# Optimization experiments

Measured on AMD Instinct MI355X. Metric: run time of the kernel, lower is better.

The kernel has to match this reference:

```python
import jax, jax.numpy as jnp
import numpy as np
from jax import lax

_MS_SSIM_WEIGHTS = [0.0448, 0.2856, 0.3001, 0.2363, 0.1333]
LEVELS = 5
WINDOW_SIZE = 11
SIGMA = 1.5
DATA_RANGE = 2.0


def _gaussian_kernel(size, sigma, channels):
    x = jnp.arange(size, dtype=jnp.float32) - size // 2
    g = jnp.exp(-x ** 2 / (2.0 * sigma ** 2))
    g = g / g.sum()
    k2d = jnp.outer(g, g)  # [size, size]
    # depthwise kernel: [C, 1, size, size] (OIHW with feature_group_count=C)
    return jnp.broadcast_to(k2d[None, None], (channels, 1, size, size))


def _depthwise_conv(x, kernel, pad):
    C = x.shape[1]
    return lax.conv_general_dilated(
        x, kernel,
        window_strides=(1, 1),
        padding=[(pad, pad), (pad, pad)],
        dimension_numbers=('NCHW', 'OIHW', 'NCHW'),
        feature_group_count=C)


def _avg_pool2(x):
    s = lax.reduce_window(x, 0.0, lax.add, (1, 1, 2, 2), (1, 1, 2, 2), 'VALID')
    return s * 0.25


def _ssim(x, y, window_size=WINDOW_SIZE, sigma=SIGMA, data_range=DATA_RANGE):
    K1, K2 = 0.01, 0.03
    C1 = (K1 * data_range) ** 2
    C2 = (K2 * data_range) ** 2
    kernel = _gaussian_kernel(window_size, sigma, x.shape[1])
    pad = window_size // 2
    mu1 = _depthwise_conv(x, kernel, pad)
    mu2 = _depthwise_conv(y, kernel, pad)
    mu1_sq = mu1 * mu1
    mu2_sq = mu2 * mu2
    mu1_mu2 = mu1 * mu2
    sig1_sq = _depthwise_conv(x * x, kernel, pad) - mu1_sq
    sig2_sq = _depthwise_conv(y * y, kernel, pad) - mu2_sq
    sig12 = _depthwise_conv(x * y, kernel, pad) - mu1_mu2
    num = (2.0 * mu1_mu2 + C1) * (2.0 * sig12 + C2)
    den = (mu1_sq + mu2_sq + C1) * (sig1_sq + sig2_sq + C2)
    ssim_map = num / (den + 1e-8)
    return ssim_map.mean()


def setup_inputs() -> dict:
    key = jax.random.key(0)
    k1, k2 = jax.random.split(key)
    pred = jax.random.normal(k1, (16, 3, 512, 512), dtype=jnp.float32)
    target = jax.random.normal(k2, (16, 3, 512, 512), dtype=jnp.float32)
    return {"pred": pred, "target": target}


def reference(pred, target):
    weights = jnp.asarray(_MS_SSIM_WEIGHTS[:LEVELS], dtype=jnp.float32)
    weights = weights / weights.sum()
    ms_ssim_val = jnp.zeros((), dtype=jnp.float32)
    x, y = pred, target
    for i in range(LEVELS):
        s = _ssim(x, y)
        ms_ssim_val = ms_ssim_val + weights[i] * s
        if i < LEVELS - 1:
            x = _avg_pool2(x)
            y = _avg_pool2(y)
    return 1.0 - ms_ssim_val
```

## Files before the change

kernel.cpp:

```cpp
#include <hip/hip_runtime.h>


#define TW 64
#define NIMG 48
#define P2 63
#define P1 62
#define NSLOT 256
#define SSTRIDE 16

typedef float v2f __attribute__((ext_vector_type(2)));

template <int TH>
__global__ __launch_bounds__(256, 2) void ssim_level_kernel(
    const float* __restrict__ x, const float* __restrict__ y,
    long imgStride, int rowStride,
    float* __restrict__ dsx, float* __restrict__ dsy,
    long dsImgStride, int dsRowStride,
    const float* __restrict__ zpad,
    float* __restrict__ slots, int H, int W, int pad, int do_ds)
{
    constexpr int HHALO = TH + 10;
    constexpr int RPT   = TH / 4;

    const float G[11] = {
        0.00102839f, 0.00759877f, 0.03600077f, 0.10936069f, 0.21300539f,
        0.26601173f, 0.21300539f, 0.10936069f, 0.03600077f, 0.00759877f,
        0.00102839f};
    const float C1 = 4.0e-4f;
    const float C2 = 3.6e-3f;

    __shared__ __align__(16) v2f   sm01[HHALO * P2];
    __shared__ __align__(16) v2f   sm23[HHALO * P2];
    __shared__ __align__(16) float sm4 [HHALO * P1];

    const int t   = threadIdx.x;
    const int img = blockIdx.z;
    const int C0  = blockIdx.x * TW;
    const int R0  = blockIdx.y * TH;
    const float* xi = x + (long)img * imgStride;
    const float* yi = y + (long)img * imgStride;

    if (do_ds) {
        const int dsW = W >> 1, dsH = H >> 1;
        const long dbase = (long)img * dsImgStride;
        for (int i = t; i < (TH / 2) * 32; i += 256) {
            const int dr = i >> 5, dc = i & 31;
            const int gr2 = (R0 >> 1) + dr;
            const int gc2 = (C0 >> 1) + dc;
            if (gr2 < dsH && gc2 < dsW) {
                const float* sx = xi + (long)(2 * gr2) * rowStride + 2 * gc2;
                const float* sy = yi + (long)(2 * gr2) * rowStride + 2 * gc2;
                const float2 a0 = *reinterpret_cast<const float2*>(sx);
                const float2 a1 = *reinterpret_cast<const float2*>(sx + rowStride);
                const float2 b0 = *reinterpret_cast<const float2*>(sy);
                const float2 b1 = *reinterpret_cast<const float2*>(sy + rowStride);
                const long o = dbase + (long)gr2 * dsRowStride + gc2;
                dsx[o] = 0.25f * (a0.x + a0.y + a1.x + a1.y);
                dsy[o] = 0.25f * (b0.x + b0.y + b1.x + b1.y);
            }
            if (gr2 < dsH && dc < 8) {
                if (blockIdx.x == 0) {
                    const long o = dbase + (long)gr2 * dsRowStride + (dc - 8);
                    dsx[o] = 0.0f; dsy[o] = 0.0f;
                }
                if (blockIdx.x == gridDim.x - 1) {
                    const long o = dbase + (long)gr2 * dsRowStride + (dsW + dc);
                    dsx[o] = 0.0f; dsy[o] = 0.0f;
                }
            }
        }
    }

    const bool fastp = pad || ((C0 >= 8) && (C0 + TW + 8 <= W));
    for (int s = t; s < HHALO * 8; s += 256) {
        const int r  = s % HHALO;
        const int q  = s / HHALO;
        const int gr = R0 + r - 5;
        const bool rok = ((unsigned)gr < (unsigned)H);
        const int gc0 = C0 + (q << 3) - 8;

        float xv[24], yv[24];
        if (fastp) {
            const float* px = rok ? (xi + (long)gr * rowStride + gc0) : zpad;
            const float* py = rok ? (yi + (long)gr * rowStride + gc0) : zpad;
#pragma unroll
            for (int v = 0; v < 6; ++v) {
                const float4 a = reinterpret_cast<const float4*>(px)[v];
                const float4 b = reinterpret_cast<const float4*>(py)[v];
                xv[4 * v + 0] = a.x; xv[4 * v + 1] = a.y;
                xv[4 * v + 2] = a.z; xv[4 * v + 3] = a.w;
                yv[4 * v + 0] = b.x; yv[4 * v + 1] = b.y;
                yv[4 * v + 2] = b.z; yv[4 * v + 3] = b.w;
            }
        } else {
            const float* xrow = xi + (long)gr * rowStride;
            const float* yrow = yi + (long)gr * rowStride;
#pragma unroll
            for (int k = 3; k < 21; ++k) {
                const int gc = gc0 + k;
                const bool ok = rok && ((unsigned)gc < (unsigned)W);
                xv[k] = ok ? xrow[gc] : 0.0f;
                yv[k] = ok ? yrow[gc] : 0.0f;
            }
        }

        v2f w2[18]; float xy[18];
#pragma unroll
        for (int k = 0; k < 18; ++k) {
            const float a = xv[k + 3], b = yv[k + 3];
            v2f w; w.x = a * a; w.y = b * b;
            w2[k] = w; xy[k] = a * b;
        }

        const int cb = (q << 3);
#pragma unroll
        for (int j = 0; j < 8; ++j) {
            v2f s01 = {0.f, 0.f}, s23 = {0.f, 0.f};
            float s4 = 0.f;
#pragma unroll
            for (int k = 0; k < 11; ++k) {
                const float g = G[k];
                v2f w; w.x = xv[j + k + 3]; w.y = yv[j + k + 3];
                s01 += w * g;
                s23 += w2[j + k] * g;
                s4   = fmaf(g, xy[j + k], s4);
            }
            sm01[r * P2 + cb + j] = s01;
            sm23[r * P2 + cb + j] = s23;
            sm4 [r * P1 + cb + j] = s4;
        }
    }
    __syncthreads();

    const int c   = t & 63;
    const int rr0 = (t >> 6) * RPT;
    v2f acc01[RPT], acc23[RPT];
    float acc4[RPT];
    {
        v2f hv[RPT + 10];
#pragma unroll
        for (int k = 0; k < RPT + 10; ++k) hv[k] = sm01[(rr0 + k) * P2 + c];
#pragma unroll
        for (int i = 0; i < RPT; ++i) {
            v2f a = {0.f, 0.f};
#pragma unroll
            for (int k = 0; k < 11; ++k) a += hv[i + k] * G[k];
            acc01[i] = a;
        }
#pragma unroll
        for (int k = 0; k < RPT + 10; ++k) hv[k] = sm23[(rr0 + k) * P2 + c];
#pragma unroll
        for (int i = 0; i < RPT; ++i) {
            v2f a = {0.f, 0.f};
#pragma unroll
            for (int k = 0; k < 11; ++k) a += hv[i + k] * G[k];
            acc23[i] = a;
        }
    }
    {
        float hs[RPT + 10];
#pragma unroll
        for (int k = 0; k < RPT + 10; ++k) hs[k] = sm4[(rr0 + k) * P1 + c];
#pragma unroll
        for (int i = 0; i < RPT; ++i) {
            float a = 0.f;
#pragma unroll
            for (int k = 0; k < 11; ++k) a = fmaf(G[k], hs[i + k], a);
            acc4[i] = a;
        }
    }

    float local = 0.f;
    const int gc = C0 + c;
#pragma unroll
    for (int i = 0; i < RPT; ++i) {
        const int gr2 = R0 + rr0 + i;
        if (gr2 < H && gc < W) {
            const float mu1 = acc01[i].x, mu2 = acc01[i].y;
            const float mu1s = mu1 * mu1, mu2s = mu2 * mu2, m12 = mu1 * mu2;
            const float s1  = acc23[i].x - mu1s;
            const float s2  = acc23[i].y - mu2s;
            const float s12 = acc4[i] - m12;
            const float num = (2.f * m12 + C1) * (2.f * s12 + C2);
            const float den = (mu1s + mu2s + C1) * (s1 + s2 + C2);
            local += num * __builtin_amdgcn_rcpf(den + 1e-8f);
        }
    }

#pragma unroll
    for (int off = 32; off > 0; off >>= 1) local += __shfl_down(local, off, 64);
    if ((t & 63) == 0) {
        const int bid = (blockIdx.z * gridDim.y + blockIdx.y) * gridDim.x + blockIdx.x;
        const int slot = ((bid << 2) | (t >> 6)) & (NSLOT - 1);
        atomicAdd(slots + slot * SSTRIDE, local);
    }
}

__global__ void finalize_kernel(const float* __restrict__ slots,
                                float* __restrict__ out)
{
    const int t = threadIdx.x;
    const float w[5] = {0.0448f, 0.2856f, 0.3001f, 0.2363f, 0.1333f};
    const float wsum = w[0] + w[1] + w[2] + w[3] + w[4];
    float acc = 0.f;
#pragma unroll
    for (int lvl = 0; lvl < 5; ++lvl) {
        const int d = 512 >> lvl;
        const float cnt = (float)NIMG * (float)d * (float)d;
        acc += (w[lvl] / wsum) / cnt * slots[(lvl * NSLOT + t) * SSTRIDE];
    }
#pragma unroll
    for (int off = 32; off > 0; off >>= 1) acc += __shfl_down(acc, off, 64);
    __shared__ float p[4];
    if ((t & 63) == 0) p[t >> 6] = acc;
    __syncthreads();
    if (t == 0) out[0] = 1.0f - (p[0] + p[1] + p[2] + p[3]);
}

extern "C" void kernel_launch(void* const* d_in, const int* in_sizes, int n_in,
                              void* d_out, int out_size, void* d_ws, size_t ws_size,
                              hipStream_t stream)
{
    const float* pred = (const float*)d_in[0];
    const float* targ = (const float*)d_in[1];
    float* out = (float*)d_out;
    float* ws  = (float*)d_ws;

    const long S1 = 256L * 272, S2 = 128L * 144, S3 = 64L * 80, S4 = 32L * 48;

    float* slots = ws;
    float* zpad  = slots + 5 * NSLOT * SSTRIDE;
    float* x1 = zpad + 640;
    float* y1 = x1 + NIMG * S1;
    float* x2 = y1 + NIMG * S1;
    float* y2 = x2 + NIMG * S2;
    float* x3 = y2 + NIMG * S2;
    float* y3 = x3 + NIMG * S3;
    float* x4 = y3 + NIMG * S3;
    float* y4 = x4 + NIMG * S4;

    hipMemsetAsync(ws, 0, (size_t)(5 * NSLOT * SSTRIDE + 640) * sizeof(float), stream);

    { dim3 g(8, 16, NIMG);
      ssim_level_kernel<32><<<g, 256, 0, stream>>>(pred, targ, 512L * 512, 512,
          x1 + 8, y1 + 8, S1, 272, zpad, slots + 0 * NSLOT * SSTRIDE, 512, 512, 0, 1); }
    { dim3 g(4, 8, NIMG);
      ssim_level_kernel<32><<<g, 256, 0, stream>>>(x1 + 8, y1 + 8, S1, 272,
          x2 + 8, y2 + 8, S2, 144, zpad, slots + 1 * NSLOT * SSTRIDE, 256, 256, 1, 1); }
    { dim3 g(2, 16, NIMG);
      ssim_level_kernel<8><<<g, 256, 0, stream>>>(x2 + 8, y2 + 8, S2, 144,
          x3 + 8, y3 + 8, S3, 80, zpad, slots + 2 * NSLOT * SSTRIDE, 128, 128, 1, 1); }
    { dim3 g(1, 8, NIMG);
      ssim_level_kernel<8><<<g, 256, 0, stream>>>(x3 + 8, y3 + 8, S3, 80,
          x4 + 8, y4 + 8, S4, 48, zpad, slots + 3 * NSLOT * SSTRIDE, 64, 64, 1, 1); }
    { dim3 g(1, 4, NIMG);
      ssim_level_kernel<8><<<g, 256, 0, stream>>>(x4 + 8, y4 + 8, S4, 48,
          nullptr, nullptr, 0, 0, zpad, slots + 4 * NSLOT * SSTRIDE, 32, 32, 1, 0); }

    finalize_kernel<<<1, 256, 0, stream>>>(slots, out);
}
```

Baseline: 283.6 us.

## Add rolling-window SSIM kernel with ring-buffer horizontal pass for top two levels

```diff
diff --git a/kernel.cpp b/kernel.cpp
--- a/kernel.cpp
+++ b/kernel.cpp
@@ -3,12 +3,230 @@
 
 #define TW 64
 #define NIMG 48
+#define WIN 42
+#define PQ  64
+#define P4  65
 #define P2 63
 #define P1 62
 #define NSLOT 256
 #define SSTRIDE 16
 
 typedef float v2f __attribute__((ext_vector_type(2)));
+typedef float v4f __attribute__((ext_vector_type(4)));
+
+__device__ __forceinline__ void h_load(
+    const float* __restrict__ xi, const float* __restrict__ yi,
+    const float* __restrict__ zpad, int gr, int gc0, int H, int W,
+    bool fastp, int rowStride, float* xv, float* yv)
+{
+    const bool rok = ((unsigned)gr < (unsigned)H);
+    if (fastp) {
+        const float* px = rok ? (xi + (long)gr * rowStride + gc0) : zpad;
+        const float* py = rok ? (yi + (long)gr * rowStride + gc0) : zpad;
+#pragma unroll
+        for (int v = 0; v < 6; ++v) {
+            const float4 a = reinterpret_cast<const float4*>(px)[v];
+            const float4 b = reinterpret_cast<const float4*>(py)[v];
+            xv[4*v+0]=a.x; xv[4*v+1]=a.y; xv[4*v+2]=a.z; xv[4*v+3]=a.w;
+            yv[4*v+0]=b.x; yv[4*v+1]=b.y; yv[4*v+2]=b.z; yv[4*v+3]=b.w;
+        }
+    } else {
+        const float* xrow = xi + (long)gr * rowStride;
+        const float* yrow = yi + (long)gr * rowStride;
+#pragma unroll
+        for (int k = 3; k < 21; ++k) {
+            const int gc = gc0 + k;
+            const bool ok = rok && ((unsigned)gc < (unsigned)W);
+            xv[k] = ok ? xrow[gc] : 0.0f;
+            yv[k] = ok ? yrow[gc] : 0.0f;
+        }
+    }
+}
+
+__device__ __forceinline__ void h_conv_write(
+    const float* xv, const float* yv, v4f* smA, float* smB,
+    int slot, int cb, const float* G)
+{
+    v2f s01[8], s23[8];
+    float s4[8];
+#pragma unroll
+    for (int j = 0; j < 8; ++j) {
+        s01[j] = {0.f, 0.f}; s23[j] = {0.f, 0.f}; s4[j] = 0.f;
+    }
+#pragma unroll
+    for (int m = 0; m < 18; ++m) {
+        const float a = xv[m+3], b = yv[m+3];
+        v2f w;  w.x  = a;   w.y  = b;
+        v2f w2; w2.x = a*a; w2.y = b*b;
+        const float ab = a * b;
+#pragma unroll
+        for (int j = 0; j < 8; ++j) {
+            if (j <= m && m - j <= 10) {
+                const float g = G[m - j];
+                s01[j] += w * g;
+                s23[j] += w2 * g;
+                s4[j] = fmaf(g, ab, s4[j]);
+            }
+        }
+    }
+    const int u = slot & 31;
+#pragma unroll
+    for (int j = 0; j < 8; ++j) {
+        v4f o; o.x = s01[j].x; o.y = s01[j].y; o.z = s23[j].x; o.w = s23[j].y;
+        smA[slot * PQ + ((cb + j) ^ u)] = o;
+        smB[slot * P4 + cb + j] = s4[j];
+    }
+}
+
+template <int NSUB>
+__global__ __launch_bounds__(256, 3) void ssim_rolling_kernel(
+    const float* __restrict__ x, const float* __restrict__ y,
+    long imgStride, int rowStride,
+    float* __restrict__ dsx, float* __restrict__ dsy,
+    long dsImgStride, int dsRowStride,
+    const float* __restrict__ zpad,
+    float* __restrict__ slots, int H, int W, int pad, int do_ds)
+{
+    const float G[11] = {
+        0.00102839f, 0.00759877f, 0.03600077f, 0.10936069f, 0.21300539f,
+        0.26601173f, 0.21300539f, 0.10936069f, 0.03600077f, 0.00759877f,
+        0.00102839f};
+    const float C1 = 4.0e-4f;
+    const float C2 = 3.6e-3f;
+
+    __shared__ __align__(16) v4f smA[WIN * PQ];
+    __shared__ float             smB[WIN * P4];
+
+    const int t   = threadIdx.x;
+    const int img = blockIdx.z;
+    const int C0  = blockIdx.x * TW;
+    const int S0  = blockIdx.y * (NSUB * 32);
+    const float* xi = x + (long)img * imgStride;
+    const float* yi = y + (long)img * imgStride;
+    const bool fastp = pad || ((C0 >= 8) && (C0 + TW + 8 <= W));
+
+    for (int s = t; s < WIN * 8; s += 256) {
+        const int r = s % WIN, q = s / WIN;
+        float pxv[24], pyv[24];
+        h_load(xi, yi, zpad, S0 + r - 5, C0 + (q << 3) - 8, H, W, fastp,
+               rowStride, pxv, pyv);
+        h_conv_write(pxv, pyv, smA, smB, r, q << 3, G);
+    }
+    __syncthreads();
+
+    const int c   = t & 63;
+    const int rr0 = (t >> 6) * 8;
+    const int hr  = t & 31, hq = t >> 5;
+    const int hgc0 = C0 + (hq << 3) - 8;
+    int wslot = hr;
+    int vb    = rr0;
+    float local = 0.f;
+    const int dsW = W >> 1, dsH = H >> 1;
+    const long dbase = (long)img * dsImgStride;
+
+    float xv[24], yv[24];
+
+    for (int tt = 0; tt < NSUB; ++tt) {
+        const int R0 = S0 + 32 * tt;
+
+        if (tt < NSUB - 1)
+            h_load(xi, yi, zpad, R0 + 37 + hr, hgc0, H, W, fastp, rowStride,
+                   xv, yv);
+
+        float2 pa0[2], pa1[2], pb0[2], pb1[2];
+        if (do_ds) {
+#pragma unroll
+            for (int ii = 0; ii < 2; ++ii) {
+                const int i  = t + (ii << 8);
+                const int dr = i >> 5, dc = i & 31;
+                const int gr2 = (R0 >> 1) + dr, gc2 = (C0 >> 1) + dc;
+                if (gr2 < dsH && gc2 < dsW) {
+                    const float* sx = xi + (long)(2*gr2) * rowStride + 2*gc2;
+                    const float* sy = yi + (long)(2*gr2) * rowStride + 2*gc2;
+                    pa0[ii] = *reinterpret_cast<const float2*>(sx);
+                    pa1[ii] = *reinterpret_cast<const float2*>(sx + rowStride);
+                    pb0[ii] = *reinterpret_cast<const float2*>(sy);
+                    pb1[ii] = *reinterpret_cast<const float2*>(sy + rowStride);
+                }
+            }
+        }
+
+        v4f accA[8]; float acc4[8];
+#pragma unroll
+        for (int i = 0; i < 8; ++i) {
+            accA[i] = {0.f, 0.f, 0.f, 0.f}; acc4[i] = 0.f;
+        }
+        int sl = __builtin_amdgcn_readfirstlane(vb);
+#pragma unroll
+        for (int k = 0; k < 18; ++k) {
+            const v4f  h  = smA[sl * PQ + (c ^ (sl & 31))];
+            const float hb = smB[sl * P4 + c];
+#pragma unroll
+            for (int i = 0; i < 8; ++i) {
+                if (i <= k && k - i <= 10) {
+                    const float g = G[k - i];
+                    accA[i] += h * g;
+                    acc4[i] = fmaf(g, hb, acc4[i]);
+                }
+            }
+            sl = (sl + 1 == WIN) ? 0 : sl + 1;
+        }
+#pragma unroll
+        for (int i = 0; i < 8; ++i) {
+            const int gr2 = R0 + rr0 + i;
+            const int gc  = C0 + c;
+            if (gr2 < H && gc < W) {
+                const float mu1 = accA[i].x, mu2 = accA[i].y;
+                const float mu1s = mu1*mu1, mu2s = mu2*mu2, m12 = mu1*mu2;
+                const float s1  = accA[i].z - mu1s;
+                const float s2  = accA[i].w - mu2s;
+                const float s12 = acc4[i] - m12;
+                const float num = (2.f * m12 + C1) * (2.f * s12 + C2);
+                const float den = (mu1s + mu2s + C1) * (s1 + s2 + C2);
+                local += num * __builtin_amdgcn_rcpf(den + 1e-8f);
+            }
+        }
+        __syncthreads();
+
+        if (do_ds) {
+#pragma unroll
+            for (int ii = 0; ii < 2; ++ii) {
+                const int i  = t + (ii << 8);
+                const int dr = i >> 5, dc = i & 31;
+                const int gr2 = (R0 >> 1) + dr, gc2 = (C0 >> 1) + dc;
+                if (gr2 < dsH && gc2 < dsW) {
+                    const long o = dbase + (long)gr2 * dsRowStride + gc2;
+                    dsx[o] = 0.25f*(pa0[ii].x+pa0[ii].y+pa1[ii].x+pa1[ii].y);
+                    dsy[o] = 0.25f*(pb0[ii].x+pb0[ii].y+pb1[ii].x+pb1[ii].y);
+                }
+                if (gr2 < dsH && dc < 8) {
+                    if (blockIdx.x == 0) {
+                        const long o = dbase + (long)gr2 * dsRowStride + (dc - 8);
+                        dsx[o] = 0.0f; dsy[o] = 0.0f;
+                    }
+                    if (blockIdx.x == gridDim.x - 1) {
+                        const long o = dbase + (long)gr2 * dsRowStride + (dsW + dc);
+                        dsx[o] = 0.0f; dsy[o] = 0.0f;
+                    }
+                }
+            }
+        }
+        if (tt < NSUB - 1)
+            h_conv_write(xv, yv, smA, smB, wslot, hq << 3, G);
+        __syncthreads();
+
+        wslot += 32; if (wslot >= WIN) wslot -= WIN;
+        vb    += 32; if (vb    >= WIN) vb    -= WIN;
+    }
+
+#pragma unroll
+    for (int off = 32; off > 0; off >>= 1) local += __shfl_down(local, off, 64);
+    if ((t & 63) == 0) {
+        const int bid = (blockIdx.z * gridDim.y + blockIdx.y) * gridDim.x + blockIdx.x;
+        const int slot = ((bid << 2) | (t >> 6)) & (NSLOT - 1);
+        atomicAdd(slots + slot * SSTRIDE, local);
+    }
+}
 
 template <int TH>
 __global__ __launch_bounds__(256, 2) void ssim_level_kernel(
@@ -241,11 +459,11 @@
 
     hipMemsetAsync(ws, 0, (size_t)(5 * NSLOT * SSTRIDE + 640) * sizeof(float), stream);
 
-    { dim3 g(8, 16, NIMG);
-      ssim_level_kernel<32><<<g, 256, 0, stream>>>(pred, targ, 512L * 512, 512,
+    { dim3 g(8, 4, NIMG);
+      ssim_rolling_kernel<4><<<g, 256, 0, stream>>>(pred, targ, 512L * 512, 512,
           x1 + 8, y1 + 8, S1, 272, zpad, slots + 0 * NSLOT * SSTRIDE, 512, 512, 0, 1); }
-    { dim3 g(4, 8, NIMG);
-      ssim_level_kernel<32><<<g, 256, 0, stream>>>(x1 + 8, y1 + 8, S1, 272,
+    { dim3 g(4, 4, NIMG);
+      ssim_rolling_kernel<2><<<g, 256, 0, stream>>>(x1 + 8, y1 + 8, S1, 272,
           x2 + 8, y2 + 8, S2, 144, zpad, slots + 1 * NSLOT * SSTRIDE, 256, 256, 1, 1); }
     { dim3 g(2, 16, NIMG);
       ssim_level_kernel<8><<<g, 256, 0, stream>>>(x2 + 8, y2 + 8, S2, 144,
```

Result: slower. 419.0 us (+47.7%).
